# Kernel optimization log

Measured on AMD Instinct MI355X. Metric: run time of the kernel, lower is better.

## Reference

```python
import jax, jax.numpy as jnp
import numpy as np

VOCAB = 50400
D_MODEL = 4096
SHARDS = 8
PER_SHARD = VOCAB // SHARDS  # 6300
B, S = 8, 2048


def setup_inputs() -> dict:
    key = jax.random.key(0)
    k1, k2, k3 = jax.random.split(key, 3)
    x = jax.random.randint(k1, (B, S), 0, VOCAB, dtype=jnp.int64) if jax.config.jax_enable_x64 else jax.random.randint(k1, (B, S), 0, VOCAB, dtype=jnp.int32)
    # Per-shard Linear weights W_s: [in_dim_per_shard, out_dim], stddev 1/sqrt(in_dim)
    W = jax.random.normal(k2, (SHARDS, PER_SHARD, D_MODEL), dtype=jnp.float32) * (1.0 / np.sqrt(VOCAB))
    b = jax.random.normal(k3, (SHARDS, D_MODEL), dtype=jnp.float32) * 0.02
    return {"x": x, "W": W, "b": b}


def reference(x, W, b):
    # Original per shard s: onehot(x vs shard-s vocab slice) @ W_s + b_s, then pmean over shards.
    # Each token id hits exactly one shard's slice, so:
    #   pmean_s(onehot_s @ W_s + b_s) = (gather(concat_s W_s, x) + sum_s b_s) / shards
    shards, per_shard, out_dim = W.shape
    W_full = W.reshape(shards * per_shard, out_dim)  # [vocab, d_model]
    tok = x.reshape(-1)                               # [B*S]
    out = jnp.take(W_full, tok, axis=0) + jnp.sum(b, axis=0)  # [B*S, d_model]
    return out / shards
```

## Files before the change

### kernel.cpp

```cpp
#include <hip/hip_runtime.h>
#include <hip/hip_bf16.h>


#define D_MODEL 4096
#define SHARDS 8

typedef float f32x4 __attribute__((ext_vector_type(4)));

__global__ void bias_sum_kernel(const float* __restrict__ b, float* __restrict__ bs) {
    int d = blockIdx.x * blockDim.x + threadIdx.x;
    if (d < D_MODEL) {
        float s = 0.0f;
#pragma unroll
        for (int i = 0; i < SHARDS; ++i) s += b[i * D_MODEL + d];
        bs[d] = s;
    }
}

__global__ __launch_bounds__(256) void gather_kernel(const int* __restrict__ tok,
                                                     const float* __restrict__ W,
                                                     const float* __restrict__ bs,
                                                     float* __restrict__ out) {
    const int t = blockIdx.x;
    const int tid = threadIdx.x;
    const int row = tok[t];

    const f32x4* wrow = reinterpret_cast<const f32x4*>(W) + (size_t)row * (D_MODEL / 4);
    const f32x4* bs4  = reinterpret_cast<const f32x4*>(bs);
    f32x4*       orow = reinterpret_cast<f32x4*>(out) + (size_t)t * (D_MODEL / 4);

#pragma unroll
    for (int j = 0; j < 4; ++j) {
        f32x4 w  = wrow[tid + j * 256];
        f32x4 bv = bs4[tid + j * 256];
        orow[tid + j * 256] = (w + bv) * 0.125f;
    }
}

extern "C" void kernel_launch(void* const* d_in, const int* in_sizes, int n_in,
                              void* d_out, int out_size, void* d_ws, size_t ws_size,
                              hipStream_t stream) {
    const int*   tok = (const int*)d_in[0];
    const float* W   = (const float*)d_in[1];
    const float* b   = (const float*)d_in[2];
    float*       out = (float*)d_out;
    float*       bs  = (float*)d_ws;

    const int ntok = in_sizes[0];

    bias_sum_kernel<<<(D_MODEL + 255) / 256, 256, 0, stream>>>(b, bs);
    gather_kernel<<<ntok, 256, 0, stream>>>(tok, W, bs, out);
}
```

Measured before the change: 106.0 us.

## Fuse bias reduction into gather kernel with multi-token blocks and row prefetch

Removes the separate bias-sum kernel by having each block reduce the shard biases into registers. Each block now handles 8 tokens and prefetches the next token's weight row while storing the current one. The aim is to cut a launch and the workspace round trip, and to overlap loads with stores. In exchange, every block re-reads all shard biases and the grid has fewer blocks.

```diff
diff --git a/kernel.cpp b/kernel.cpp
--- a/kernel.cpp
+++ b/kernel.cpp
@@ -4,36 +4,58 @@
 
 #define D_MODEL 4096
 #define SHARDS 8
+#define TPB 8
 
 typedef float f32x4 __attribute__((ext_vector_type(4)));
 
-__global__ void bias_sum_kernel(const float* __restrict__ b, float* __restrict__ bs) {
-    int d = blockIdx.x * blockDim.x + threadIdx.x;
-    if (d < D_MODEL) {
-        float s = 0.0f;
-#pragma unroll
-        for (int i = 0; i < SHARDS; ++i) s += b[i * D_MODEL + d];
-        bs[d] = s;
-    }
-}
+__global__ __launch_bounds__(256) void fused_gather_kernel(const int* __restrict__ tok,
+                                                           const float* __restrict__ W,
+                                                           const float* __restrict__ b,
+                                                           float* __restrict__ out,
+                                                           int ntok) {
+    const int tid = threadIdx.x;
+    const int base = blockIdx.x * TPB;
 
-__global__ __launch_bounds__(256) void gather_kernel(const int* __restrict__ tok,
-                                                     const float* __restrict__ W,
-                                                     const float* __restrict__ bs,
-                                                     float* __restrict__ out) {
-    const int t = blockIdx.x;
-    const int tid = threadIdx.x;
-    const int row = tok[t];
-
-    const f32x4* wrow = reinterpret_cast<const f32x4*>(W) + (size_t)row * (D_MODEL / 4);
-    const f32x4* bs4  = reinterpret_cast<const f32x4*>(bs);
-    f32x4*       orow = reinterpret_cast<f32x4*>(out) + (size_t)t * (D_MODEL / 4);
-
+    f32x4 bias[4];
 #pragma unroll
     for (int j = 0; j < 4; ++j) {
-        f32x4 w  = wrow[tid + j * 256];
-        f32x4 bv = bs4[tid + j * 256];
-        orow[tid + j * 256] = (w + bv) * 0.125f;
+        f32x4 s = {0.f, 0.f, 0.f, 0.f};
+#pragma unroll
+        for (int sh = 0; sh < SHARDS; ++sh)
+            s += reinterpret_cast<const f32x4*>(b + sh * D_MODEL)[tid + j * 256];
+        bias[j] = s;
+    }
+
+    const f32x4* W4   = reinterpret_cast<const f32x4*>(W);
+    f32x4*       out4 = reinterpret_cast<f32x4*>(out);
+
+    int row = tok[base];
+    f32x4 cur[4];
+    {
+        const f32x4* wr = W4 + (size_t)row * (D_MODEL / 4);
+#pragma unroll
+        for (int j = 0; j < 4; ++j) cur[j] = wr[tid + j * 256];
+    }
+
+#pragma unroll 1
+    for (int i = 0; i < TPB; ++i) {
+        f32x4 nxt[4];
+        const bool have_next = (i + 1 < TPB) && (base + i + 1 < ntok);
+        if (have_next) {
+            const int nrow = tok[base + i + 1];
+            const f32x4* wn = W4 + (size_t)nrow * (D_MODEL / 4);
+#pragma unroll
+            for (int j = 0; j < 4; ++j) nxt[j] = wn[tid + j * 256];
+        }
+        if (base + i < ntok) {
+            f32x4* orow = out4 + (size_t)(base + i) * (D_MODEL / 4);
+#pragma unroll
+            for (int j = 0; j < 4; ++j) orow[tid + j * 256] = (cur[j] + bias[j]) * 0.125f;
+        }
+        if (have_next) {
+#pragma unroll
+            for (int j = 0; j < 4; ++j) cur[j] = nxt[j];
+        }
     }
 }
 
@@ -44,10 +66,9 @@
     const float* W   = (const float*)d_in[1];
     const float* b   = (const float*)d_in[2];
     float*       out = (float*)d_out;
-    float*       bs  = (float*)d_ws;
 
     const int ntok = in_sizes[0];
+    const int grid = (ntok + TPB - 1) / TPB;
 
-    bias_sum_kernel<<<(D_MODEL + 255) / 256, 256, 0, stream>>>(b, bs);
-    gather_kernel<<<ntok, 256, 0, stream>>>(tok, W, bs, out);
+    fused_gather_kernel<<<grid, 256, 0, stream>>>(tok, W, b, out, ntok);
 }
```

New measurement: 107.5 us. Within noise of the previous version (+1.4%).
